# Optimization experiments

Hardware: AMD Instinct MI355X
Metric: run time of the kernel (lower is better)

The kernel has to match this reference:

```python
import jax, jax.numpy as jnp
import numpy as np

B, NF, D = 8192, 64, 128


def setup_inputs() -> dict:
    key = jax.random.key(0)
    k1, k2, k3, k4 = jax.random.split(key, 4)
    F = jax.random.normal(k1, (B, NF, D), dtype=jnp.float32)
    # interaction weight tensor (num_fields, num_fields, embedding_dim)
    W = jax.random.normal(k2, (NF, NF, D), dtype=jnp.float32) * 0.05
    # torch Linear weights (out_features, in_features); y = x @ W.T
    K_w = jax.random.normal(k3, (D, D), dtype=jnp.float32) * (1.0 / np.sqrt(D))
    Q_w = jax.random.normal(k4, (D, D), dtype=jnp.float32) * (1.0 / np.sqrt(D))
    return {"F": F, "W": W, "K_w": K_w, "Q_w": Q_w}


def reference(F, W, K_w, Q_w):
    # K(F): torch Linear without bias -> F @ K_w.T, shape [B, NF, D]
    Kf = jnp.einsum('bjd,ed->bje', F, K_w)
    # S = bmm(F, K(F)^T) -> [B, NF, NF]
    S = jnp.einsum('bid,bjd->bij', F, Kf)
    # (S.unsqueeze(-1) * W).sum(dim=2) without materializing [B,NF,NF,D]
    out = jnp.einsum('bij,ijd->bid', S, W)
    # residual: Q(F)
    out = out + jnp.einsum('bid,ed->bie', F, Q_w)
    return out
```

## Files before the change

### kernel.cpp

```cpp
#include <hip/hip_runtime.h>
#include <stdint.h>

typedef _Float16 f16x8 __attribute__((ext_vector_type(8)));
typedef _Float16 f16x4 __attribute__((ext_vector_type(4)));
typedef float    f32x4 __attribute__((ext_vector_type(4)));

#define NFIELD 64
#define DIM    128
#define BTOT   8192
#define NB     8

__device__ __forceinline__ f16x8 cvt8(float4 a, float4 b) {
  f16x8 h;
  h[0] = (_Float16)a.x; h[1] = (_Float16)a.y; h[2] = (_Float16)a.z; h[3] = (_Float16)a.w;
  h[4] = (_Float16)b.x; h[5] = (_Float16)b.y; h[6] = (_Float16)b.z; h[7] = (_Float16)b.w;
  return h;
}

__global__ void prep_kernel(const float* __restrict__ W,
                            const float* __restrict__ Kw,
                            const float* __restrict__ Qw,
                            _Float16* __restrict__ Wt,
                            _Float16* __restrict__ Kh,
                            _Float16* __restrict__ Qh) {
  const int blk = blockIdx.x, t = threadIdx.x;
  if (blk < NFIELD) {
    const float* Wi = W + (size_t)blk * NFIELD * DIM;
    _Float16* Wo = Wt + (size_t)blk * DIM * NFIELD;
    for (int idx = t; idx < DIM * NFIELD; idx += 256) {
      int d = idx >> 6, j = idx & 63;
      Wo[idx] = (_Float16)Wi[j * DIM + d];
    }
  } else if (blk == NFIELD) {
    for (int idx = t; idx < DIM * DIM; idx += 256) Kh[idx] = (_Float16)Kw[idx];
  } else {
    for (int idx = t; idx < DIM * DIM; idx += 256) Qh[idx] = (_Float16)Qw[idx];
  }
}

__global__ __launch_bounds__(256, 2)
void s_kernel(const float* __restrict__ F,
              const _Float16* __restrict__ Kh,
              _Float16* __restrict__ Sg, int c0) {
  __shared__ __attribute__((aligned(16))) _Float16 sF[2][64 * 128];
  __shared__ __attribute__((aligned(16))) _Float16 sKf[64 * 128];
  __shared__ __attribute__((aligned(16))) _Float16 sS[2][64 * 64];
  const int t = threadIdx.x;
  const int lane = t & 63, wave = t >> 6;
  const int l15 = lane & 15, quad = lane >> 4;
  const int bbase = blockIdx.x * NB;

  f16x8 kh[2][4];
#pragma unroll
  for (int eh = 0; eh < 2; ++eh)
#pragma unroll
    for (int kt = 0; kt < 4; ++kt)
      kh[eh][kt] = *(const f16x8*)(Kh + ((wave * 2 + eh) * 16 + l15) * DIM + kt * 32 + quad * 8);

  float4 fr[8];
  {
    const float4* Fb4 = (const float4*)(F + (size_t)(c0 + bbase) * (NFIELD * DIM));
#pragma unroll
    for (int k = 0; k < 4; ++k) {
      int u = t + k * 256;
      fr[2 * k]     = Fb4[2 * u];
      fr[2 * k + 1] = Fb4[2 * u + 1];
    }
#pragma unroll
    for (int k = 0; k < 4; ++k) {
      int u = t + k * 256;
      int row = u >> 4, c8 = u & 15;
      *(f16x8*)((char*)&sF[0][0] + row * 256 + ((c8 * 16) ^ ((row & 7) << 4))) =
          cvt8(fr[2 * k], fr[2 * k + 1]);
    }
  }
  {
    const float4* Fb4 = (const float4*)(F + (size_t)(c0 + bbase + 1) * (NFIELD * DIM));
#pragma unroll
    for (int k = 0; k < 4; ++k) {
      int u = t + k * 256;
      fr[2 * k]     = Fb4[2 * u];
      fr[2 * k + 1] = Fb4[2 * u + 1];
    }
  }
  __syncthreads();

  for (int bi = 0; bi < NB; ++bi) {
    const int cur = bi & 1;
    const _Float16* sFc = &sF[cur][0];

    f16x8 afc[4][4];
#pragma unroll
    for (int jt = 0; jt < 4; ++jt)
#pragma unroll
      for (int kt = 0; kt < 4; ++kt) {
        int row = jt * 16 + l15;
        afc[jt][kt] = *(const f16x8*)((const char*)sFc + row * 256 +
                                      ((kt * 64 + quad * 16) ^ ((row & 7) << 4)));
      }
    f32x4 aKf[4][2];
#pragma unroll
    for (int jt = 0; jt < 4; ++jt) {
      aKf[jt][0] = (f32x4){0.f, 0.f, 0.f, 0.f};
      aKf[jt][1] = (f32x4){0.f, 0.f, 0.f, 0.f};
    }
#pragma unroll
    for (int jt = 0; jt < 4; ++jt)
#pragma unroll
      for (int kt = 0; kt < 4; ++kt) {
        aKf[jt][0] = __builtin_amdgcn_mfma_f32_16x16x32_f16(afc[jt][kt], kh[0][kt], aKf[jt][0], 0, 0, 0);
        aKf[jt][1] = __builtin_amdgcn_mfma_f32_16x16x32_f16(afc[jt][kt], kh[1][kt], aKf[jt][1], 0, 0, 0);
      }
#pragma unroll
    for (int jt = 0; jt < 4; ++jt)
#pragma unroll
      for (int eh = 0; eh < 2; ++eh) {
        int e = (wave * 2 + eh) * 16 + l15;
#pragma unroll
        for (int r = 0; r < 4; ++r) {
          int j = jt * 16 + quad * 4 + r;
          *(_Float16*)((char*)sKf + j * 256 + ((e * 2) ^ ((j & 7) << 4))) =
              (_Float16)aKf[jt][eh][r];
        }
      }
    if (bi + 1 < NB) {
#pragma unroll
      for (int k = 0; k < 4; ++k) {
        int u = t + k * 256;
        int row = u >> 4, c8 = u & 15;
        *(f16x8*)((char*)&sF[cur ^ 1][0] + row * 256 + ((c8 * 16) ^ ((row & 7) << 4))) =
            cvt8(fr[2 * k], fr[2 * k + 1]);
      }
    }
    __syncthreads();

    if (bi + 2 < NB) {
      const float4* Fb4 = (const float4*)(F + (size_t)(c0 + bbase + bi + 2) * (NFIELD * DIM));
#pragma unroll
      for (int k = 0; k < 4; ++k) {
        int u = t + k * 256;
        fr[2 * k]     = Fb4[2 * u];
        fr[2 * k + 1] = Fb4[2 * u + 1];
      }
    }

    if (bi > 0) {
      _Float16* dst = Sg + (size_t)(bbase + bi - 1) * (NFIELD * NFIELD);
#pragma unroll
      for (int k = 0; k < 2; ++k) {
        int idx = t + k * 256;
        int si = idx >> 3, j8 = idx & 7;
        f16x8 v = *(const f16x8*)((const char*)&sS[cur ^ 1][0] + si * 128 +
                                  ((j8 * 16) ^ ((si & 7) << 4)));
        *(f16x8*)(dst + si * 64 + j8 * 8) = v;
      }
    }

    f16x8 bS[4];
#pragma unroll
    for (int kt = 0; kt < 4; ++kt) {
      int row = wave * 16 + l15;
      bS[kt] = *(const f16x8*)((const char*)sKf + row * 256 +
                               ((kt * 64 + quad * 16) ^ ((row & 7) << 4)));
    }
    f32x4 aS[4];
#pragma unroll
    for (int it = 0; it < 4; ++it) aS[it] = (f32x4){0.f, 0.f, 0.f, 0.f};
#pragma unroll
    for (int it = 0; it < 4; ++it)
#pragma unroll
      for (int kt = 0; kt < 4; ++kt)
        aS[it] = __builtin_amdgcn_mfma_f32_16x16x32_f16(afc[it][kt], bS[kt], aS[it], 0, 0, 0);
#pragma unroll
    for (int it = 0; it < 4; ++it)
#pragma unroll
      for (int r = 0; r < 4; ++r) {
        int si = it * 16 + quad * 4 + r, j = wave * 16 + l15;
        *(_Float16*)((char*)&sS[cur][0] + si * 128 + ((j * 2) ^ ((si & 7) << 4))) =
            (_Float16)aS[it][r];
      }
    __syncthreads();
  }
  {
    const int cur = (NB - 1) & 1;
    _Float16* dst = Sg + (size_t)(bbase + NB - 1) * (NFIELD * NFIELD);
#pragma unroll
    for (int k = 0; k < 2; ++k) {
      int idx = t + k * 256;
      int si = idx >> 3, j8 = idx & 7;
      f16x8 v = *(const f16x8*)((const char*)&sS[cur][0] + si * 128 +
                                ((j8 * 16) ^ ((si & 7) << 4)));
      *(f16x8*)(dst + si * 64 + j8 * 8) = v;
    }
  }
}

__global__ __launch_bounds__(256, 2)
void out_kernel(const float* __restrict__ F,
                const _Float16* __restrict__ Sg,
                const _Float16* __restrict__ Wt,
                const _Float16* __restrict__ Qh,
                float* __restrict__ Out, int c0) {
  __shared__ __attribute__((aligned(16))) _Float16 sBt[128 * 200];
  const int i = blockIdx.y;
  const int t = threadIdx.x;
  const int lane = t & 63, wave = t >> 6;
  const int l15 = lane & 15, quad = lane >> 4;

  const f16x8* wp = (const f16x8*)(Wt + (size_t)i * DIM * NFIELD);
#pragma unroll
  for (int k = 0; k < 4; ++k) {
    int idx = t + k * 256;
    int d = idx >> 3, jw = idx & 7;
    *(f16x8*)&sBt[d * 200 + jw * 8] = wp[idx];
  }
  const f16x8* qp = (const f16x8*)Qh;
#pragma unroll
  for (int k = 0; k < 8; ++k) {
    int idx = t + k * 256;
    int d = idx >> 4, ew = idx & 15;
    *(f16x8*)&sBt[d * 200 + 64 + ew * 8] = qp[idx];
  }

  const int bl0 = blockIdx.x * 128;
  f16x8 aS[2][2];
  float4 fr[2][8];
#pragma unroll
  for (int mi = 0; mi < 2; ++mi) {
    const int bl = bl0 + (wave * 2 + mi) * 16 + l15;
#pragma unroll
    for (int kt = 0; kt < 2; ++kt)
      aS[mi][kt] = *(const f16x8*)(Sg + (size_t)bl * 4096 + i * 64 + kt * 32 + quad * 8);
    const float* fp = F + ((size_t)(c0 + bl) * NFIELD + i) * DIM + quad * 8;
#pragma unroll
    for (int kt = 0; kt < 4; ++kt) {
      fr[mi][2 * kt]     = *(const float4*)(fp + kt * 32);
      fr[mi][2 * kt + 1] = *(const float4*)(fp + kt * 32 + 4);
    }
  }
  __syncthreads();

  f32x4 acc[2][8];
#pragma unroll
  for (int mi = 0; mi < 2; ++mi)
#pragma unroll
    for (int nt = 0; nt < 8; ++nt) acc[mi][nt] = (f32x4){0.f, 0.f, 0.f, 0.f};

#pragma unroll
  for (int kt = 0; kt < 6; ++kt) {
    f16x8 af[2];
#pragma unroll
    for (int mi = 0; mi < 2; ++mi) {
      if (kt < 2) af[mi] = aS[mi][kt];
      else        af[mi] = cvt8(fr[mi][2 * (kt - 2)], fr[mi][2 * (kt - 2) + 1]);
    }
#pragma unroll
    for (int nt = 0; nt < 8; ++nt) {
      f16x8 bf = *(const f16x8*)&sBt[(nt * 16 + l15) * 200 + kt * 32 + quad * 8];
      acc[0][nt] = __builtin_amdgcn_mfma_f32_16x16x32_f16(af[0], bf, acc[0][nt], 0, 0, 0);
      acc[1][nt] = __builtin_amdgcn_mfma_f32_16x16x32_f16(af[1], bf, acc[1][nt], 0, 0, 0);
    }
  }

#pragma unroll
  for (int mi = 0; mi < 2; ++mi) {
    const int blr = bl0 + (wave * 2 + mi) * 16 + quad * 4;
#pragma unroll
    for (int nt = 0; nt < 8; ++nt) {
      const int d = nt * 16 + l15;
#pragma unroll
      for (int r = 0; r < 4; ++r) {
        const size_t gb = (size_t)(c0 + blr + r);
        Out[(gb * NFIELD + i) * DIM + d] = acc[mi][nt][r];
      }
    }
  }
}

extern "C" void kernel_launch(void* const* d_in, const int* in_sizes, int n_in,
                              void* d_out, int out_size, void* d_ws, size_t ws_size,
                              hipStream_t stream) {
  const float* F  = (const float*)d_in[0];
  const float* W  = (const float*)d_in[1];
  const float* Kw = (const float*)d_in[2];
  const float* Qw = (const float*)d_in[3];
  float* Out = (float*)d_out;

  _Float16* Wt = (_Float16*)d_ws;
  _Float16* Kh = Wt + (size_t)NFIELD * DIM * NFIELD;
  _Float16* Qh = Kh + DIM * DIM;
  _Float16* Sg = Qh + DIM * DIM;
  const size_t fixed_bytes = ((size_t)NFIELD * DIM * NFIELD + 2 * DIM * DIM) * sizeof(_Float16);
  size_t avail = (ws_size > fixed_bytes) ? (ws_size - fixed_bytes) : 0;
  int CB = BTOT;
  while (CB > 128 && (size_t)CB * NFIELD * NFIELD * sizeof(_Float16) > avail) CB >>= 1;

  prep_kernel<<<dim3(NFIELD + 2), 256, 0, stream>>>(W, Kw, Qw, Wt, Kh, Qh);
  for (int c0 = 0; c0 < BTOT; c0 += CB) {
    s_kernel<<<dim3(CB / NB), 256, 0, stream>>>(F, Kh, Sg, c0);
    out_kernel<<<dim3(CB / 128, NFIELD), 256, 0, stream>>>(F, Sg, Wt, Qh, Out, c0);
  }
}
```

Before: 606.4 us.

## Restructure S kernel to cut registers and LDS, raise occupancy, widen prep

The S kernel no longer keeps all 16 F fragments in registers across both GEMMs. It reloads them from LDS per tile and swaps MFMA operand order so Kf and S results are written as vectorized f16x4 stores. The sS staging buffer is dropped and S goes straight to global memory, which frees LDS. Launch bounds are raised to 3 blocks per SM to lift occupancy. The prep kernel is split over four times as many blocks with vectorized K/Q conversion, at the cost of extra LDS reads and uncoalesced direct global stores of S.

```diff
diff --git a/kernel.cpp b/kernel.cpp
--- a/kernel.cpp
+++ b/kernel.cpp
@@ -24,27 +24,37 @@
                             _Float16* __restrict__ Kh,
                             _Float16* __restrict__ Qh) {
   const int blk = blockIdx.x, t = threadIdx.x;
-  if (blk < NFIELD) {
-    const float* Wi = W + (size_t)blk * NFIELD * DIM;
-    _Float16* Wo = Wt + (size_t)blk * DIM * NFIELD;
-    for (int idx = t; idx < DIM * NFIELD; idx += 256) {
-      int d = idx >> 6, j = idx & 63;
-      Wo[idx] = (_Float16)Wi[j * DIM + d];
-    }
-  } else if (blk == NFIELD) {
-    for (int idx = t; idx < DIM * DIM; idx += 256) Kh[idx] = (_Float16)Kw[idx];
+  if (blk < NFIELD * 4) {
+    const int i = blk >> 2, dq = blk & 3;
+    const float* Wi = W + (size_t)i * NFIELD * DIM;
+    _Float16* Wo = Wt + (size_t)i * DIM * NFIELD;
+    for (int idx = t; idx < 32 * NFIELD; idx += 256) {
+      int d = dq * 32 + (idx >> 6), j = idx & 63;
+      Wo[d * 64 + j] = (_Float16)Wi[j * DIM + d];
+    }
+  } else if (blk == NFIELD * 4) {
+    const float4* src = (const float4*)Kw;
+    for (int u = t; u < DIM * DIM / 4; u += 256) {
+      float4 v = src[u];
+      f16x4 h; h[0] = (_Float16)v.x; h[1] = (_Float16)v.y; h[2] = (_Float16)v.z; h[3] = (_Float16)v.w;
+      *(f16x4*)&Kh[u * 4] = h;
+    }
   } else {
-    for (int idx = t; idx < DIM * DIM; idx += 256) Qh[idx] = (_Float16)Qw[idx];
-  }
-}
-
-__global__ __launch_bounds__(256, 2)
+    const float4* src = (const float4*)Qw;
+    for (int u = t; u < DIM * DIM / 4; u += 256) {
+      float4 v = src[u];
+      f16x4 h; h[0] = (_Float16)v.x; h[1] = (_Float16)v.y; h[2] = (_Float16)v.z; h[3] = (_Float16)v.w;
+      *(f16x4*)&Qh[u * 4] = h;
+    }
+  }
+}
+
+__global__ __launch_bounds__(256, 3)
 void s_kernel(const float* __restrict__ F,
               const _Float16* __restrict__ Kh,
               _Float16* __restrict__ Sg, int c0) {
   __shared__ __attribute__((aligned(16))) _Float16 sF[2][64 * 128];
   __shared__ __attribute__((aligned(16))) _Float16 sKf[64 * 128];
-  __shared__ __attribute__((aligned(16))) _Float16 sS[2][64 * 64];
   const int t = threadIdx.x;
   const int lane = t & 63, wave = t >> 6;
   const int l15 = lane & 15, quad = lane >> 4;
@@ -87,42 +97,31 @@
 
   for (int bi = 0; bi < NB; ++bi) {
     const int cur = bi & 1;
-    const _Float16* sFc = &sF[cur][0];
-
-    f16x8 afc[4][4];
-#pragma unroll
-    for (int jt = 0; jt < 4; ++jt)
+    const char* sFc = (const char*)&sF[cur][0];
+
+#pragma unroll
+    for (int jt = 0; jt < 4; ++jt) {
+      f16x8 bf[4];
 #pragma unroll
       for (int kt = 0; kt < 4; ++kt) {
         int row = jt * 16 + l15;
-        afc[jt][kt] = *(const f16x8*)((const char*)sFc + row * 256 +
-                                      ((kt * 64 + quad * 16) ^ ((row & 7) << 4)));
-      }
-    f32x4 aKf[4][2];
-#pragma unroll
-    for (int jt = 0; jt < 4; ++jt) {
-      aKf[jt][0] = (f32x4){0.f, 0.f, 0.f, 0.f};
-      aKf[jt][1] = (f32x4){0.f, 0.f, 0.f, 0.f};
-    }
-#pragma unroll
-    for (int jt = 0; jt < 4; ++jt)
+        bf[kt] = *(const f16x8*)(sFc + row * 256 + ((kt * 64 + quad * 16) ^ ((row & 7) << 4)));
+      }
+      f32x4 a0 = {0.f, 0.f, 0.f, 0.f}, a1 = {0.f, 0.f, 0.f, 0.f};
 #pragma unroll
       for (int kt = 0; kt < 4; ++kt) {
-        aKf[jt][0] = __builtin_amdgcn_mfma_f32_16x16x32_f16(afc[jt][kt], kh[0][kt], aKf[jt][0], 0, 0, 0);
-        aKf[jt][1] = __builtin_amdgcn_mfma_f32_16x16x32_f16(afc[jt][kt], kh[1][kt], aKf[jt][1], 0, 0, 0);
-      }
-#pragma unroll
-    for (int jt = 0; jt < 4; ++jt)
-#pragma unroll
-      for (int eh = 0; eh < 2; ++eh) {
-        int e = (wave * 2 + eh) * 16 + l15;
-#pragma unroll
-        for (int r = 0; r < 4; ++r) {
-          int j = jt * 16 + quad * 4 + r;
-          *(_Float16*)((char*)sKf + j * 256 + ((e * 2) ^ ((j & 7) << 4))) =
-              (_Float16)aKf[jt][eh][r];
-        }
-      }
+        a0 = __builtin_amdgcn_mfma_f32_16x16x32_f16(kh[0][kt], bf[kt], a0, 0, 0, 0);
+        a1 = __builtin_amdgcn_mfma_f32_16x16x32_f16(kh[1][kt], bf[kt], a1, 0, 0, 0);
+      }
+      const int j = jt * 16 + l15;
+      const int eb0 = (wave * 2) * 32 + quad * 8;
+      f16x4 h0, h1;
+#pragma unroll
+      for (int r = 0; r < 4; ++r) { h0[r] = (_Float16)a0[r]; h1[r] = (_Float16)a1[r]; }
+      *(f16x4*)((char*)sKf + j * 256 + ((eb0)      ^ ((j & 7) << 4))) = h0;
+      *(f16x4*)((char*)sKf + j * 256 + ((eb0 + 32) ^ ((j & 7) << 4))) = h1;
+    }
+
     if (bi + 1 < NB) {
 #pragma unroll
       for (int k = 0; k < 4; ++k) {
@@ -131,67 +130,44 @@
         *(f16x8*)((char*)&sF[cur ^ 1][0] + row * 256 + ((c8 * 16) ^ ((row & 7) << 4))) =
             cvt8(fr[2 * k], fr[2 * k + 1]);
       }
+      if (bi + 2 < NB) {
+        const float4* Fb4 = (const float4*)(F + (size_t)(c0 + bbase + bi + 2) * (NFIELD * DIM));
+#pragma unroll
+        for (int k = 0; k < 4; ++k) {
+          int u = t + k * 256;
+          fr[2 * k]     = Fb4[2 * u];
+          fr[2 * k + 1] = Fb4[2 * u + 1];
+        }
+      }
     }
     __syncthreads();
 
-    if (bi + 2 < NB) {
-      const float4* Fb4 = (const float4*)(F + (size_t)(c0 + bbase + bi + 2) * (NFIELD * DIM));
-#pragma unroll
-      for (int k = 0; k < 4; ++k) {
-        int u = t + k * 256;
-        fr[2 * k]     = Fb4[2 * u];
-        fr[2 * k + 1] = Fb4[2 * u + 1];
-      }
-    }
-
-    if (bi > 0) {
-      _Float16* dst = Sg + (size_t)(bbase + bi - 1) * (NFIELD * NFIELD);
-#pragma unroll
-      for (int k = 0; k < 2; ++k) {
-        int idx = t + k * 256;
-        int si = idx >> 3, j8 = idx & 7;
-        f16x8 v = *(const f16x8*)((const char*)&sS[cur ^ 1][0] + si * 128 +
-                                  ((j8 * 16) ^ ((si & 7) << 4)));
-        *(f16x8*)(dst + si * 64 + j8 * 8) = v;
-      }
-    }
-
-    f16x8 bS[4];
+    f16x8 kfA[4];
 #pragma unroll
     for (int kt = 0; kt < 4; ++kt) {
       int row = wave * 16 + l15;
-      bS[kt] = *(const f16x8*)((const char*)sKf + row * 256 +
-                               ((kt * 64 + quad * 16) ^ ((row & 7) << 4)));
-    }
-    f32x4 aS[4];
-#pragma unroll
-    for (int it = 0; it < 4; ++it) aS[it] = (f32x4){0.f, 0.f, 0.f, 0.f};
-#pragma unroll
-    for (int it = 0; it < 4; ++it)
+      kfA[kt] = *(const f16x8*)((const char*)sKf + row * 256 +
+                                ((kt * 64 + quad * 16) ^ ((row & 7) << 4)));
+    }
+    _Float16* dst = Sg + (size_t)(bbase + bi) * (NFIELD * NFIELD);
+#pragma unroll
+    for (int it = 0; it < 4; ++it) {
+      f16x8 bf[4];
+#pragma unroll
+      for (int kt = 0; kt < 4; ++kt) {
+        int row = it * 16 + l15;
+        bf[kt] = *(const f16x8*)(sFc + row * 256 + ((kt * 64 + quad * 16) ^ ((row & 7) << 4)));
+      }
+      f32x4 acc = {0.f, 0.f, 0.f, 0.f};
 #pragma unroll
       for (int kt = 0; kt < 4; ++kt)
-        aS[it] = __builtin_amdgcn_mfma_f32_16x16x32_f16(afc[it][kt], bS[kt], aS[it], 0, 0, 0);
-#pragma unroll
-    for (int it = 0; it < 4; ++it)
-#pragma unroll
-      for (int r = 0; r < 4; ++r) {
-        int si = it * 16 + quad * 4 + r, j = wave * 16 + l15;
-        *(_Float16*)((char*)&sS[cur][0] + si * 128 + ((j * 2) ^ ((si & 7) << 4))) =
-            (_Float16)aS[it][r];
-      }
+        acc = __builtin_amdgcn_mfma_f32_16x16x32_f16(kfA[kt], bf[kt], acc, 0, 0, 0);
+      f16x4 sv;
+#pragma unroll
+      for (int r = 0; r < 4; ++r) sv[r] = (_Float16)acc[r];
+      *(f16x4*)(dst + (it * 16 + l15) * 64 + wave * 16 + quad * 4) = sv;
+    }
     __syncthreads();
-  }
-  {
-    const int cur = (NB - 1) & 1;
-    _Float16* dst = Sg + (size_t)(bbase + NB - 1) * (NFIELD * NFIELD);
-#pragma unroll
-    for (int k = 0; k < 2; ++k) {
-      int idx = t + k * 256;
-      int si = idx >> 3, j8 = idx & 7;
-      f16x8 v = *(const f16x8*)((const char*)&sS[cur][0] + si * 128 +
-                                ((j8 * 16) ^ ((si & 7) << 4)));
-      *(f16x8*)(dst + si * 64 + j8 * 8) = v;
-    }
   }
 }
 
@@ -295,7 +271,7 @@
   int CB = BTOT;
   while (CB > 128 && (size_t)CB * NFIELD * NFIELD * sizeof(_Float16) > avail) CB >>= 1;
 
-  prep_kernel<<<dim3(NFIELD + 2), 256, 0, stream>>>(W, Kw, Qw, Wt, Kh, Qh);
+  prep_kernel<<<dim3(NFIELD * 4 + 2), 256, 0, stream>>>(W, Kw, Qw, Wt, Kh, Qh);
   for (int c0 = 0; c0 < BTOT; c0 += CB) {
     s_kernel<<<dim3(CB / NB), 256, 0, stream>>>(F, Kh, Sg, c0);
     out_kernel<<<dim3(CB / 128, NFIELD), 256, 0, stream>>>(F, Sg, Wt, Qh, Out, c0);
```

After: 556.5 us. 8.2% less time.
